# Optimization experiments

Hardware: AMD Instinct MI355X
Metric: run time of the kernel (lower is better)

Reference implementation:

```python
import jax, jax.numpy as jnp
import numpy as np

EPS = 1e-5  # torch nn.LayerNorm default eps
N_SUBJECTS = 16


def _gelu(x):
    # torch nn.GELU default = exact erf formulation
    return jax.nn.gelu(x, approximate=False)


def setup_inputs() -> dict:
    key = jax.random.key(0)
    ks = jax.random.split(key, 8)
    B, D = 131072, 512
    x = jax.random.normal(ks[0], (B, D), dtype=jnp.float32)
    groups = jax.random.randint(ks[1], (B,), 0, N_SUBJECTS, dtype=jnp.int32)
    # LayerNorm affine params: rows 0..15 subject-specific, row 16 = default_norm
    gammas = jnp.ones((N_SUBJECTS + 1, D), dtype=jnp.float32)
    betas = jnp.zeros((N_SUBJECTS + 1, D), dtype=jnp.float32)
    # Domain classifier MLP (xavier-uniform weights, zero biases)
    def xavier(k, fan_in, fan_out):
        lim = np.sqrt(6.0 / (fan_in + fan_out)).astype(np.float32)
        return jax.random.uniform(k, (fan_in, fan_out), dtype=jnp.float32,
                                  minval=-lim, maxval=lim)
    W1 = xavier(ks[2], D, 256); b1 = jnp.zeros((256,), jnp.float32)
    W2 = xavier(ks[3], 256, 128); b2 = jnp.zeros((128,), jnp.float32)
    W3 = xavier(ks[4], 128, N_SUBJECTS); b3 = jnp.zeros((N_SUBJECTS,), jnp.float32)
    return {"x": x, "groups": groups, "gammas": gammas, "betas": betas,
            "W1": W1, "b1": b1, "W2": W2, "b2": b2, "W3": W3, "b3": b3}


def _subject_layernorm(x, groups, gammas, betas):
    # Fused per-row LayerNorm with per-subject affine params.
    # Out-of-range subject ids (>= N_SUBJECTS or < 0) use the default row (index N_SUBJECTS).
    valid = (groups >= 0) & (groups < N_SUBJECTS)
    idx = jnp.where(valid, groups, N_SUBJECTS)
    g = gammas[idx]  # (B, D)
    b = betas[idx]   # (B, D)
    mu = jnp.mean(x, axis=-1, keepdims=True)
    var = jnp.mean(jnp.square(x - mu), axis=-1, keepdims=True)  # biased, as torch LN
    xn = (x - mu) * jax.lax.rsqrt(var + EPS)
    return xn * g + b


def _domain_classifier(x, W1, b1, W2, b2, W3, b3):
    # Dropout is identity in eval mode
    h = _gelu(x @ W1 + b1)
    h = _gelu(h @ W2 + b2)
    return h @ W3 + b3


def reference(x, groups, gammas, betas, W1, b1, W2, b2, W3, b3):
    # gradient reversal is identity in forward
    domain_logits = _domain_classifier(x, W1, b1, W2, b2, W3, b3)
    normalized_x = _subject_layernorm(x, groups, gammas, betas)
    return (normalized_x, domain_logits)
```

## Files before the change

### kernel.cpp

```cpp
#include <hip/hip_runtime.h>
#include <hip/hip_bf16.h>
#include <stdint.h>

#define NSUB 16

typedef short  bf16x8 __attribute__((ext_vector_type(8)));
typedef float  f32x4  __attribute__((ext_vector_type(4)));
typedef unsigned int u32x4 __attribute__((ext_vector_type(4)));

__device__ __forceinline__ float gelu_exact(float x){
  return 0.5f * x * (1.0f + erff(x * 0.70710678118654752440f));
}

__device__ __forceinline__ unsigned short f2bf(float f){
  union { float f; uint32_t u; } v; v.f = f;
  uint32_t u = v.u;
  return (unsigned short)((u + 0x7FFFu + ((u >> 16) & 1u)) >> 16);
}

__device__ __forceinline__ unsigned int pk2(float lo, float hi){
  union { __hip_bfloat162 b; unsigned int u; } c;
  c.b = __float22bfloat162_rn(make_float2(lo, hi));
  return c.u;
}

__device__ __forceinline__ bf16x8 as_bf(u32x4 v){
  union { u32x4 u; bf16x8 b; } c; c.u = v; return c.b;
}

__device__ __forceinline__ float bflo(unsigned int u){
  union { unsigned int u; float f; } c; c.u = u << 16; return c.f;
}
__device__ __forceinline__ float bfhi(unsigned int u){
  union { unsigned int u; float f; } c; c.u = u & 0xffff0000u; return c.f;
}

__global__ __launch_bounds__(256) void wconv_kernel(
    const float* __restrict__ W1, const float* __restrict__ W2, const float* __restrict__ W3,
    unsigned short* __restrict__ W1f, unsigned short* __restrict__ W2f, unsigned short* __restrict__ W3f){
  int t = blockIdx.x * 256 + threadIdx.x;
  if (t < 131072){
    int n = t >> 9, k = t & 511;
    int lane = ((k >> 3) & 3) * 16 + (n & 15);
    int idx = (((k >> 5) * 16 + (n >> 4)) * 64 + lane) * 8 + (k & 7);
    W1f[idx] = f2bf(W1[k*256 + n]);
  } else if (t < 131072 + 32768){
    int i = t - 131072; int n = i >> 8, k = i & 255;
    int lane = ((k >> 3) & 3) * 16 + (n & 15);
    int idx = (((k >> 5) * 8 + (n >> 4)) * 64 + lane) * 8 + (k & 7);
    W2f[idx] = f2bf(W2[k*128 + n]);
  } else if (t < 131072 + 32768 + 2048){
    int i = t - (131072 + 32768); int n = i >> 7, k = i & 127;
    int lane = ((k >> 3) & 3) * 16 + n;
    int idx = ((k >> 5) * 64 + lane) * 8 + (k & 7);
    W3f[idx] = f2bf(W3[k*16 + n]);
  }
}

__global__ __launch_bounds__(256) void fused_kernel(
    const float* __restrict__ x, const int* __restrict__ groups,
    const float* __restrict__ gammas, const float* __restrict__ betas,
    const unsigned short* __restrict__ W1f, const float* __restrict__ b1,
    const unsigned short* __restrict__ W2f, const float* __restrict__ b2,
    const unsigned short* __restrict__ W3f, const float* __restrict__ b3,
    float* __restrict__ ln_out, float* __restrict__ out2){
  __shared__ __align__(16) uint8_t smem[32768];
  constexpr int OFF_H2 = 16384;

  const int tid  = threadIdx.x;
  const int wave = tid >> 6;
  const int lane = tid & 63;
  const int l15  = lane & 15;
  const int g4   = lane >> 4;
  const int row0 = blockIdx.x * 32;

  const int sr  = tid >> 3;
  const int sc  = tid & 7;
  const int swz = (sr & 7) << 4;
  const int wb  = (sc*16) ^ swz;
  uint8_t* xrow = smem + sr*1024;
  const float* xg = x + (size_t)(row0 + sr)*512 + sc*8;

  float s = 0.f, q = 0.f;
  #pragma unroll
  for (int t = 0; t < 8; ++t){
    f32x4 v0 = *(const f32x4*)(xg + t*64);
    f32x4 v1 = *(const f32x4*)(xg + t*64 + 4);
    s += v0.x + v0.y + v0.z + v0.w + v1.x + v1.y + v1.z + v1.w;
    q += v0.x*v0.x + v0.y*v0.y + v0.z*v0.z + v0.w*v0.w
       + v1.x*v1.x + v1.y*v1.y + v1.z*v1.z + v1.w*v1.w;
    u32x4 pw;
    pw.x = pk2(v0.x, v0.y); pw.y = pk2(v0.z, v0.w);
    pw.z = pk2(v1.x, v1.y); pw.w = pk2(v1.z, v1.w);
    *(u32x4*)(xrow + t*128 + wb) = pw;
  }
  s += __shfl_xor(s, 1); s += __shfl_xor(s, 2); s += __shfl_xor(s, 4);
  q += __shfl_xor(q, 1); q += __shfl_xor(q, 2); q += __shfl_xor(q, 4);
  float mu  = s * (1.0f/512.0f);
  float var = q * (1.0f/512.0f) - mu*mu;
  float rs  = rsqrtf(var + 1e-5f);
  float nmr = -mu * rs;
  int gi   = groups[row0 + sr];
  int gidx = ((unsigned)gi < (unsigned)NSUB) ? gi : NSUB;

  float b1v[4], b2v[2], b3v;
  #pragma unroll
  for (int n = 0; n < 4; ++n) b1v[n] = b1[wave*64 + n*16 + l15];
  #pragma unroll
  for (int n = 0; n < 2; ++n) b2v[n] = b2[wave*32 + n*16 + l15];
  b3v = b3[l15];

  {
    const float* gpr = gammas + (size_t)gidx*512 + sc*8;
    const float* bpr = betas  + (size_t)gidx*512 + sc*8;
    float* op = ln_out + (size_t)(row0 + sr)*512 + sc*8;
    #pragma unroll
    for (int t = 0; t < 8; ++t){
      u32x4 pw = *(const u32x4*)(xrow + t*128 + wb);
      f32x4 g0 = *(const f32x4*)(gpr + t*64);
      f32x4 g1 = *(const f32x4*)(gpr + t*64 + 4);
      f32x4 e0 = *(const f32x4*)(bpr + t*64);
      f32x4 e1 = *(const f32x4*)(bpr + t*64 + 4);
      f32x4 o0, o1;
      o0.x = fmaf(fmaf(bflo(pw.x), rs, nmr), g0.x, e0.x);
      o0.y = fmaf(fmaf(bfhi(pw.x), rs, nmr), g0.y, e0.y);
      o0.z = fmaf(fmaf(bflo(pw.y), rs, nmr), g0.z, e0.z);
      o0.w = fmaf(fmaf(bfhi(pw.y), rs, nmr), g0.w, e0.w);
      o1.x = fmaf(fmaf(bflo(pw.z), rs, nmr), g1.x, e1.x);
      o1.y = fmaf(fmaf(bfhi(pw.z), rs, nmr), g1.y, e1.y);
      o1.z = fmaf(fmaf(bflo(pw.w), rs, nmr), g1.z, e1.z);
      o1.w = fmaf(fmaf(bfhi(pw.w), rs, nmr), g1.w, e1.w);
      *(f32x4*)(op + t*64)     = o0;
      *(f32x4*)(op + t*64 + 4) = o1;
    }
  }

  __syncthreads();

  int baseA[2][2];
  #pragma unroll
  for (int m = 0; m < 2; ++m){
    int row = m*16 + l15;
    int sw  = (row & 7) << 4;
    int bse = row*1024 + ((g4*16) ^ (sw & 0x30));
    int kx  = (row >> 2) & 1;
    baseA[m][0] = bse + ((0 ^ kx) << 6);
    baseA[m][1] = bse + ((1 ^ kx) << 6);
  }
  u32x4 braw[2][4];
  #pragma unroll
  for (int n = 0; n < 4; ++n)
    braw[0][n] = *(const u32x4*)(W1f + (size_t)(((wave*4 + n)*64 + lane)*8));
  f32x4 acc1[2][4] = {};
  #pragma unroll
  for (int g = 0; g < 16; ++g){
    if (g < 15){
      #pragma unroll
      for (int n = 0; n < 4; ++n)
        braw[(g+1)&1][n] = *(const u32x4*)(W1f + (size_t)((((g+1)*16 + wave*4 + n)*64 + lane)*8));
    }
    bf16x8 a[2];
    #pragma unroll
    for (int m = 0; m < 2; ++m)
      a[m] = *(const bf16x8*)(smem + baseA[m][g & 1] + (g >> 1)*128);
    #pragma unroll
    for (int m = 0; m < 2; ++m)
      #pragma unroll
      for (int n = 0; n < 4; ++n)
        acc1[m][n] = __builtin_amdgcn_mfma_f32_16x16x32_bf16(a[m], as_bf(braw[g & 1][n]), acc1[m][n], 0, 0, 0);
  }
  __syncthreads();

  u32x4 b2raw[2][2];
  #pragma unroll
  for (int n = 0; n < 2; ++n)
    b2raw[0][n] = *(const u32x4*)(W2f + (size_t)(((wave*2 + n)*64 + lane)*8));

  #pragma unroll
  for (int n = 0; n < 4; ++n){
    #pragma unroll
    for (int m = 0; m < 2; ++m){
      #pragma unroll
      for (int r = 0; r < 4; ++r){
        int row = m*16 + g4*4 + r;
        int col = wave*64 + n*16 + l15;
        float v = gelu_exact(acc1[m][n][r] + b1v[n]);
        *(unsigned short*)(smem + row*512 + ((col*2) ^ ((row & 7) << 4))) = f2bf(v);
      }
    }
  }
  __syncthreads();

  int baseH[2][2];
  #pragma unroll
  for (int m = 0; m < 2; ++m){
    int row = m*16 + l15;
    int sw  = (row & 7) << 4;
    int bse = row*512 + ((g4*16) ^ (sw & 0x30));
    int kx  = (row >> 2) & 1;
    baseH[m][0] = bse + ((0 ^ kx) << 6);
    baseH[m][1] = bse + ((1 ^ kx) << 6);
  }
  f32x4 acc2[2][2] = {};
  #pragma unroll
  for (int g = 0; g < 8; ++g){
    if (g < 7){
      #pragma unroll
      for (int n = 0; n < 2; ++n)
        b2raw[(g+1)&1][n] = *(const u32x4*)(W2f + (size_t)((((g+1)*8 + wave*2 + n)*64 + lane)*8));
    }
    bf16x8 a[2];
    #pragma unroll
    for (int m = 0; m < 2; ++m)
      a[m] = *(const bf16x8*)(smem + baseH[m][g & 1] + (g >> 1)*128);
    #pragma unroll
    for (int m = 0; m < 2; ++m)
      #pragma unroll
      for (int n = 0; n < 2; ++n)
        acc2[m][n] = __builtin_amdgcn_mfma_f32_16x16x32_bf16(a[m], as_bf(b2raw[g & 1][n]), acc2[m][n], 0, 0, 0);
  }

  u32x4 b3raw[4];
  #pragma unroll
  for (int ks = 0; ks < 4; ++ks)
    b3raw[ks] = *(const u32x4*)(W3f + (size_t)((ks*64 + lane)*8));

  #pragma unroll
  for (int n = 0; n < 2; ++n){
    #pragma unroll
    for (int m = 0; m < 2; ++m){
      #pragma unroll
      for (int r = 0; r < 4; ++r){
        int row = m*16 + g4*4 + r;
        int col = wave*32 + n*16 + l15;
        float v = gelu_exact(acc2[m][n][r] + b2v[n]);
        *(unsigned short*)(smem + OFF_H2 + row*256 + ((col*2) ^ ((row & 7) << 4))) = f2bf(v);
      }
    }
  }
  __syncthreads();

  int baseG[2];
  {
    int row = (wave & 1)*16 + l15;
    int sw  = (row & 7) << 4;
    int bse = OFF_H2 + row*256 + ((g4*16) ^ (sw & 0x30));
    int kx  = (row >> 2) & 1;
    baseG[0] = bse + ((0 ^ kx) << 6);
    baseG[1] = bse + ((1 ^ kx) << 6);
  }
  f32x4 acc3 = {};
  #pragma unroll
  for (int ks = 0; ks < 4; ++ks){
    bf16x8 a = *(const bf16x8*)(smem + baseG[ks & 1] + (ks >> 1)*128);
    acc3 = __builtin_amdgcn_mfma_f32_16x16x32_bf16(a, as_bf(b3raw[ks]), acc3, 0, 0, 0);
  }
  if (wave < 2){
    #pragma unroll
    for (int r = 0; r < 4; ++r){
      int grow = row0 + wave*16 + g4*4 + r;
      out2[(size_t)grow*16 + l15] = acc3[r] + b3v;
    }
  }
}

__global__ __launch_bounds__(256) void ln_kernel(
    const float* __restrict__ x, const int* __restrict__ groups,
    const float* __restrict__ gammas, const float* __restrict__ betas,
    float* __restrict__ out){
  int row  = blockIdx.x * 4 + (threadIdx.x >> 6);
  int lane = threadIdx.x & 63;
  const float4* xr = (const float4*)(x + (size_t)row * 512);
  float4 a = xr[lane];
  float4 b = xr[lane + 64];
  float s = a.x + a.y + a.z + a.w + b.x + b.y + b.z + b.w;
  float q = a.x*a.x + a.y*a.y + a.z*a.z + a.w*a.w
          + b.x*b.x + b.y*b.y + b.z*b.z + b.w*b.w;
  #pragma unroll
  for (int o = 32; o > 0; o >>= 1){
    s += __shfl_xor(s, o);
    q += __shfl_xor(q, o);
  }
  float mu  = s * (1.0f/512.0f);
  float var = q * (1.0f/512.0f) - mu*mu;
  float rs  = rsqrtf(var + 1e-5f);
  int gi = groups[row];
  int idx = ((unsigned)gi < (unsigned)NSUB) ? gi : NSUB;
  const float4* gr = (const float4*)(gammas + (size_t)idx * 512);
  const float4* br = (const float4*)(betas  + (size_t)idx * 512);
  float4 g0 = gr[lane], g1 = gr[lane + 64];
  float4 e0 = br[lane], e1 = br[lane + 64];
  float4 o0, o1;
  o0.x = (a.x - mu)*rs*g0.x + e0.x; o0.y = (a.y - mu)*rs*g0.y + e0.y;
  o0.z = (a.z - mu)*rs*g0.z + e0.z; o0.w = (a.w - mu)*rs*g0.w + e0.w;
  o1.x = (b.x - mu)*rs*g1.x + e1.x; o1.y = (b.y - mu)*rs*g1.y + e1.y;
  o1.z = (b.z - mu)*rs*g1.z + e1.z; o1.w = (b.w - mu)*rs*g1.w + e1.w;
  float4* orow = (float4*)(out + (size_t)row * 512);
  orow[lane]      = o0;
  orow[lane + 64] = o1;
}

__global__ __launch_bounds__(256) void mlp_naive(
    const float* __restrict__ x,
    const float* __restrict__ W1, const float* __restrict__ b1,
    const float* __restrict__ W2, const float* __restrict__ b2,
    const float* __restrict__ W3, const float* __restrict__ b3,
    float* __restrict__ out2){
  __shared__ float xr[512];
  __shared__ float h1[256];
  __shared__ float h2[128];
  int row = blockIdx.x, t = threadIdx.x;
  xr[t]       = x[(size_t)row*512 + t];
  xr[t + 256] = x[(size_t)row*512 + t + 256];
  __syncthreads();
  {
    float s = 0.f;
    for (int k = 0; k < 512; ++k) s += xr[k] * W1[k*256 + t];
    h1[t] = gelu_exact(s + b1[t]);
  }
  __syncthreads();
  if (t < 128){
    float s = 0.f;
    for (int k = 0; k < 256; ++k) s += h1[k] * W2[k*128 + t];
    h2[t] = gelu_exact(s + b2[t]);
  }
  __syncthreads();
  if (t < 16){
    float s = 0.f;
    for (int k = 0; k < 128; ++k) s += h2[k] * W3[k*16 + t];
    out2[(size_t)row*16 + t] = s + b3[t];
  }
}

extern "C" void kernel_launch(void* const* d_in, const int* in_sizes, int n_in,
                              void* d_out, int out_size, void* d_ws, size_t ws_size,
                              hipStream_t stream){
  const float* x      = (const float*)d_in[0];
  const int*   groups = (const int*)d_in[1];
  const float* gammas = (const float*)d_in[2];
  const float* betas  = (const float*)d_in[3];
  const float* W1 = (const float*)d_in[4];
  const float* b1 = (const float*)d_in[5];
  const float* W2 = (const float*)d_in[6];
  const float* b2 = (const float*)d_in[7];
  const float* W3 = (const float*)d_in[8];
  const float* b3 = (const float*)d_in[9];
  float* out  = (float*)d_out;
  const int B = in_sizes[0] / 512;
  float* out2 = out + (size_t)B * 512;

  const size_t ws_need = (size_t)(131072 + 32768 + 2048) * sizeof(unsigned short);
  if (ws_size >= ws_need){
    unsigned short* W1f = (unsigned short*)d_ws;
    unsigned short* W2f = W1f + 131072;
    unsigned short* W3f = W2f + 32768;
    int nconv = 131072 + 32768 + 2048;
    wconv_kernel<<<(nconv + 255)/256, 256, 0, stream>>>(W1, W2, W3, W1f, W2f, W3f);
    fused_kernel<<<B/32, 256, 0, stream>>>(x, groups, gammas, betas,
                                           W1f, b1, W2f, b2, W3f, b3, out, out2);
  } else {
    mlp_naive<<<B, 256, 0, stream>>>(x, W1, b1, W2, b2, W3, b3, out2);
    ln_kernel<<<B/4, 256, 0, stream>>>(x, groups, gammas, betas, out);
  }
}
```

Baseline: 189.2 us.

## Interleave LayerNorm output writes with first GEMM loop and use bf16 affine params

Moves the LayerNorm affine-output loop inside the first MFMA k-loop, so the per-row normalized stores overlap with matrix-core work instead of running before the barrier. Gammas and betas are now converted to bf16 in the prep kernel, which halves their gather traffic. W2 prefetch is deepened to three stages, output stores become nontemporal, and launch bounds request 4 blocks per CU. Rounding gamma and beta to bf16 adds error to the LayerNorm output. The extra register pressure from the deeper prefetch and the carried LN state may cause spills under the occupancy bound.

Result: no change. 188.1 us (-0.6%).

```diff
diff --git a/kernel.cpp b/kernel.cpp
--- a/kernel.cpp
+++ b/kernel.cpp
@@ -37,29 +37,38 @@
 
 __global__ __launch_bounds__(256) void wconv_kernel(
     const float* __restrict__ W1, const float* __restrict__ W2, const float* __restrict__ W3,
-    unsigned short* __restrict__ W1f, unsigned short* __restrict__ W2f, unsigned short* __restrict__ W3f){
+    const float* __restrict__ gammas, const float* __restrict__ betas,
+    unsigned short* __restrict__ W1f, unsigned short* __restrict__ W2f,
+    unsigned short* __restrict__ W3f, unsigned short* __restrict__ Gf,
+    unsigned short* __restrict__ Bf){
   int t = blockIdx.x * 256 + threadIdx.x;
   if (t < 131072){
     int n = t >> 9, k = t & 511;
     int lane = ((k >> 3) & 3) * 16 + (n & 15);
     int idx = (((k >> 5) * 16 + (n >> 4)) * 64 + lane) * 8 + (k & 7);
     W1f[idx] = f2bf(W1[k*256 + n]);
-  } else if (t < 131072 + 32768){
+  } else if (t < 163840){
     int i = t - 131072; int n = i >> 8, k = i & 255;
     int lane = ((k >> 3) & 3) * 16 + (n & 15);
     int idx = (((k >> 5) * 8 + (n >> 4)) * 64 + lane) * 8 + (k & 7);
     W2f[idx] = f2bf(W2[k*128 + n]);
-  } else if (t < 131072 + 32768 + 2048){
-    int i = t - (131072 + 32768); int n = i >> 7, k = i & 127;
+  } else if (t < 165888){
+    int i = t - 163840; int n = i >> 7, k = i & 127;
     int lane = ((k >> 3) & 3) * 16 + n;
     int idx = ((k >> 5) * 64 + lane) * 8 + (k & 7);
     W3f[idx] = f2bf(W3[k*16 + n]);
-  }
-}
-
-__global__ __launch_bounds__(256) void fused_kernel(
+  } else if (t < 174592){
+    int i = t - 165888;
+    Gf[i] = f2bf(gammas[i]);
+  } else if (t < 183296){
+    int i = t - 174592;
+    Bf[i] = f2bf(betas[i]);
+  }
+}
+
+__global__ __launch_bounds__(256, 4) void fused_kernel(
     const float* __restrict__ x, const int* __restrict__ groups,
-    const float* __restrict__ gammas, const float* __restrict__ betas,
+    const unsigned short* __restrict__ Gf, const unsigned short* __restrict__ Bf,
     const unsigned short* __restrict__ W1f, const float* __restrict__ b1,
     const unsigned short* __restrict__ W2f, const float* __restrict__ b2,
     const unsigned short* __restrict__ W3f, const float* __restrict__ b3,
@@ -80,6 +89,9 @@
   const int wb  = (sc*16) ^ swz;
   uint8_t* xrow = smem + sr*1024;
   const float* xg = x + (size_t)(row0 + sr)*512 + sc*8;
+
+  int gi   = groups[row0 + sr];
+  int gidx = ((unsigned)gi < (unsigned)NSUB) ? gi : NSUB;
 
   float s = 0.f, q = 0.f;
   #pragma unroll
@@ -100,8 +112,6 @@
   float var = q * (1.0f/512.0f) - mu*mu;
   float rs  = rsqrtf(var + 1e-5f);
   float nmr = -mu * rs;
-  int gi   = groups[row0 + sr];
-  int gidx = ((unsigned)gi < (unsigned)NSUB) ? gi : NSUB;
 
   float b1v[4], b2v[2], b3v;
   #pragma unroll
@@ -110,32 +120,17 @@
   for (int n = 0; n < 2; ++n) b2v[n] = b2[wave*32 + n*16 + l15];
   b3v = b3[l15];
 
-  {
-    const float* gpr = gammas + (size_t)gidx*512 + sc*8;
-    const float* bpr = betas  + (size_t)gidx*512 + sc*8;
-    float* op = ln_out + (size_t)(row0 + sr)*512 + sc*8;
-    #pragma unroll
-    for (int t = 0; t < 8; ++t){
-      u32x4 pw = *(const u32x4*)(xrow + t*128 + wb);
-      f32x4 g0 = *(const f32x4*)(gpr + t*64);
-      f32x4 g1 = *(const f32x4*)(gpr + t*64 + 4);
-      f32x4 e0 = *(const f32x4*)(bpr + t*64);
-      f32x4 e1 = *(const f32x4*)(bpr + t*64 + 4);
-      f32x4 o0, o1;
-      o0.x = fmaf(fmaf(bflo(pw.x), rs, nmr), g0.x, e0.x);
-      o0.y = fmaf(fmaf(bfhi(pw.x), rs, nmr), g0.y, e0.y);
-      o0.z = fmaf(fmaf(bflo(pw.y), rs, nmr), g0.z, e0.z);
-      o0.w = fmaf(fmaf(bfhi(pw.y), rs, nmr), g0.w, e0.w);
-      o1.x = fmaf(fmaf(bflo(pw.z), rs, nmr), g1.x, e1.x);
-      o1.y = fmaf(fmaf(bfhi(pw.z), rs, nmr), g1.y, e1.y);
-      o1.z = fmaf(fmaf(bflo(pw.w), rs, nmr), g1.z, e1.z);
-      o1.w = fmaf(fmaf(bfhi(pw.w), rs, nmr), g1.w, e1.w);
-      *(f32x4*)(op + t*64)     = o0;
-      *(f32x4*)(op + t*64 + 4) = o1;
-    }
-  }
-
-  __syncthreads();
+  const unsigned short* gam = Gf + (size_t)gidx*512 + sc*8;
+  const unsigned short* bet = Bf + (size_t)gidx*512 + sc*8;
+  float* op = ln_out + (size_t)(row0 + sr)*512 + sc*8;
+  u32x4 pwc = *(const u32x4*)(xrow + wb);
+  u32x4 ggc = *(const u32x4*)gam;
+  u32x4 bbc = *(const u32x4*)bet;
+
+  u32x4 braw[2][4];
+  #pragma unroll
+  for (int n = 0; n < 4; ++n)
+    braw[0][n] = *(const u32x4*)(W1f + (size_t)(((wave*4 + n)*64 + lane)*8));
 
   int baseA[2][2];
   #pragma unroll
@@ -147,10 +142,9 @@
     baseA[m][0] = bse + ((0 ^ kx) << 6);
     baseA[m][1] = bse + ((1 ^ kx) << 6);
   }
-  u32x4 braw[2][4];
-  #pragma unroll
-  for (int n = 0; n < 4; ++n)
-    braw[0][n] = *(const u32x4*)(W1f + (size_t)(((wave*4 + n)*64 + lane)*8));
+
+  __syncthreads();
+
   f32x4 acc1[2][4] = {};
   #pragma unroll
   for (int g = 0; g < 16; ++g){
@@ -163,18 +157,42 @@
     #pragma unroll
     for (int m = 0; m < 2; ++m)
       a[m] = *(const bf16x8*)(smem + baseA[m][g & 1] + (g >> 1)*128);
+    if (g & 1){
+      const int c = g >> 1;
+      u32x4 pwn = pwc, ggn = ggc, bbn = bbc;
+      if (c < 7){
+        pwn = *(const u32x4*)(xrow + (c+1)*128 + wb);
+        ggn = *(const u32x4*)(gam + (c+1)*64);
+        bbn = *(const u32x4*)(bet + (c+1)*64);
+      }
+      f32x4 o0, o1;
+      o0.x = fmaf(fmaf(bflo(pwc.x), rs, nmr), bflo(ggc.x), bflo(bbc.x));
+      o0.y = fmaf(fmaf(bfhi(pwc.x), rs, nmr), bfhi(ggc.x), bfhi(bbc.x));
+      o0.z = fmaf(fmaf(bflo(pwc.y), rs, nmr), bflo(ggc.y), bflo(bbc.y));
+      o0.w = fmaf(fmaf(bfhi(pwc.y), rs, nmr), bfhi(ggc.y), bfhi(bbc.y));
+      o1.x = fmaf(fmaf(bflo(pwc.z), rs, nmr), bflo(ggc.z), bflo(bbc.z));
+      o1.y = fmaf(fmaf(bfhi(pwc.z), rs, nmr), bfhi(ggc.z), bfhi(bbc.z));
+      o1.z = fmaf(fmaf(bflo(pwc.w), rs, nmr), bflo(ggc.w), bflo(bbc.w));
+      o1.w = fmaf(fmaf(bfhi(pwc.w), rs, nmr), bfhi(ggc.w), bfhi(bbc.w));
+      __builtin_nontemporal_store(o0, (f32x4*)(op + c*64));
+      __builtin_nontemporal_store(o1, (f32x4*)(op + c*64 + 4));
+      pwc = pwn; ggc = ggn; bbc = bbn;
+    }
     #pragma unroll
     for (int m = 0; m < 2; ++m)
       #pragma unroll
       for (int n = 0; n < 4; ++n)
         acc1[m][n] = __builtin_amdgcn_mfma_f32_16x16x32_bf16(a[m], as_bf(braw[g & 1][n]), acc1[m][n], 0, 0, 0);
   }
-  __syncthreads();
-
-  u32x4 b2raw[2][2];
-  #pragma unroll
-  for (int n = 0; n < 2; ++n)
-    b2raw[0][n] = *(const u32x4*)(W2f + (size_t)(((wave*2 + n)*64 + lane)*8));
+
+  u32x4 b2raw[4][2];
+  #pragma unroll
+  for (int p = 0; p < 3; ++p)
+    #pragma unroll
+    for (int n = 0; n < 2; ++n)
+      b2raw[p][n] = *(const u32x4*)(W2f + (size_t)(((p*8 + wave*2 + n)*64 + lane)*8));
+
+  __syncthreads();
 
   #pragma unroll
   for (int n = 0; n < 4; ++n){
@@ -204,10 +222,10 @@
   f32x4 acc2[2][2] = {};
   #pragma unroll
   for (int g = 0; g < 8; ++g){
-    if (g < 7){
+    if (g < 5){
       #pragma unroll
       for (int n = 0; n < 2; ++n)
-        b2raw[(g+1)&1][n] = *(const u32x4*)(W2f + (size_t)((((g+1)*8 + wave*2 + n)*64 + lane)*8));
+        b2raw[(g+3)&3][n] = *(const u32x4*)(W2f + (size_t)((((g+3)*8 + wave*2 + n)*64 + lane)*8));
     }
     bf16x8 a[2];
     #pragma unroll
@@ -217,7 +235,7 @@
     for (int m = 0; m < 2; ++m)
       #pragma unroll
       for (int n = 0; n < 2; ++n)
-        acc2[m][n] = __builtin_amdgcn_mfma_f32_16x16x32_bf16(a[m], as_bf(b2raw[g & 1][n]), acc2[m][n], 0, 0, 0);
+        acc2[m][n] = __builtin_amdgcn_mfma_f32_16x16x32_bf16(a[m], as_bf(b2raw[g & 3][n]), acc2[m][n], 0, 0, 0);
   }
 
   u32x4 b3raw[4];
@@ -259,7 +277,7 @@
     #pragma unroll
     for (int r = 0; r < 4; ++r){
       int grow = row0 + wave*16 + g4*4 + r;
-      out2[(size_t)grow*16 + l15] = acc3[r] + b3v;
+      __builtin_nontemporal_store(acc3[r] + b3v, &out2[(size_t)grow*16 + l15]);
     }
   }
 }
@@ -283,7 +301,7 @@
   }
   float mu  = s * (1.0f/512.0f);
   float var = q * (1.0f/512.0f) - mu*mu;
-  float rs  = rsqrtf(var + 1e-5f);
+  float rsq = rsqrtf(var + 1e-5f);
   int gi = groups[row];
   int idx = ((unsigned)gi < (unsigned)NSUB) ? gi : NSUB;
   const float4* gr = (const float4*)(gammas + (size_t)idx * 512);
@@ -291,10 +309,10 @@
   float4 g0 = gr[lane], g1 = gr[lane + 64];
   float4 e0 = br[lane], e1 = br[lane + 64];
   float4 o0, o1;
-  o0.x = (a.x - mu)*rs*g0.x + e0.x; o0.y = (a.y - mu)*rs*g0.y + e0.y;
-  o0.z = (a.z - mu)*rs*g0.z + e0.z; o0.w = (a.w - mu)*rs*g0.w + e0.w;
-  o1.x = (b.x - mu)*rs*g1.x + e1.x; o1.y = (b.y - mu)*rs*g1.y + e1.y;
-  o1.z = (b.z - mu)*rs*g1.z + e1.z; o1.w = (b.w - mu)*rs*g1.w + e1.w;
+  o0.x = (a.x - mu)*rsq*g0.x + e0.x; o0.y = (a.y - mu)*rsq*g0.y + e0.y;
+  o0.z = (a.z - mu)*rsq*g0.z + e0.z; o0.w = (a.w - mu)*rsq*g0.w + e0.w;
+  o1.x = (b.x - mu)*rsq*g1.x + e1.x; o1.y = (b.y - mu)*rsq*g1.y + e1.y;
+  o1.z = (b.z - mu)*rsq*g1.z + e1.z; o1.w = (b.w - mu)*rsq*g1.w + e1.w;
   float4* orow = (float4*)(out + (size_t)row * 512);
   orow[lane]      = o0;
   orow[lane + 64] = o1;
@@ -349,14 +367,17 @@
   const int B = in_sizes[0] / 512;
   float* out2 = out + (size_t)B * 512;
 
-  const size_t ws_need = (size_t)(131072 + 32768 + 2048) * sizeof(unsigned short);
+  const int n_u16 = 131072 + 32768 + 2048 + 8704 + 8704;
+  const size_t ws_need = (size_t)n_u16 * sizeof(unsigned short);
   if (ws_size >= ws_need){
     unsigned short* W1f = (unsigned short*)d_ws;
     unsigned short* W2f = W1f + 131072;
     unsigned short* W3f = W2f + 32768;
-    int nconv = 131072 + 32768 + 2048;
-    wconv_kernel<<<(nconv + 255)/256, 256, 0, stream>>>(W1, W2, W3, W1f, W2f, W3f);
-    fused_kernel<<<B/32, 256, 0, stream>>>(x, groups, gammas, betas,
+    unsigned short* Gf  = W3f + 2048;
+    unsigned short* Bf  = Gf + 8704;
+    wconv_kernel<<<(n_u16 + 255)/256, 256, 0, stream>>>(W1, W2, W3, gammas, betas,
+                                                        W1f, W2f, W3f, Gf, Bf);
+    fused_kernel<<<B/32, 256, 0, stream>>>(x, groups, Gf, Bf,
                                            W1f, b1, W2f, b2, W3f, b3, out, out2);
   } else {
     mlp_naive<<<B, 256, 0, stream>>>(x, W1, b1, W2, b2, W3, b3, out2);
```

## Halve rows per block, shrink LDS, deepen W2 prefetch, use fast GELU

Applied to the files above, without the earlier changes.

Processes 16 rows per block instead of 32, halving shared memory and per-wave accumulators so more blocks can be resident to hide memory latency. W2 fragments are prefetched three stages ahead, and the W1 prefetch is hoisted before the LayerNorm output. Exact erf GELU is replaced by a sigmoid-form tanh approximation built on exp2/rcp intrinsics. In exchange each block amortises weight loads over fewer rows, raising weight traffic, and the GELU becomes approximate.

Measured after the change: 221.4 us. +17.0%, slower.

```diff
diff --git a/kernel.cpp b/kernel.cpp
--- a/kernel.cpp
+++ b/kernel.cpp
@@ -10,6 +10,15 @@
 
 __device__ __forceinline__ float gelu_exact(float x){
   return 0.5f * x * (1.0f + erff(x * 0.70710678118654752440f));
+}
+
+__device__ __forceinline__ float gelu_fast(float x){
+  float xx = x * x;
+  float m  = fmaf(0.044715f, xx, 1.0f);
+  float a  = x * m * -2.3022084f;
+  float e  = __builtin_amdgcn_exp2f(a);
+  float r  = __builtin_amdgcn_rcpf(e + 1.0f);
+  return x * r;
 }
 
 __device__ __forceinline__ unsigned short f2bf(float f){
@@ -44,13 +53,13 @@
     int lane = ((k >> 3) & 3) * 16 + (n & 15);
     int idx = (((k >> 5) * 16 + (n >> 4)) * 64 + lane) * 8 + (k & 7);
     W1f[idx] = f2bf(W1[k*256 + n]);
-  } else if (t < 131072 + 32768){
+  } else if (t < 163840){
     int i = t - 131072; int n = i >> 8, k = i & 255;
     int lane = ((k >> 3) & 3) * 16 + (n & 15);
     int idx = (((k >> 5) * 8 + (n >> 4)) * 64 + lane) * 8 + (k & 7);
     W2f[idx] = f2bf(W2[k*128 + n]);
-  } else if (t < 131072 + 32768 + 2048){
-    int i = t - (131072 + 32768); int n = i >> 7, k = i & 127;
+  } else if (t < 165888){
+    int i = t - 163840; int n = i >> 7, k = i & 127;
     int lane = ((k >> 3) & 3) * 16 + n;
     int idx = ((k >> 5) * 64 + lane) * 8 + (k & 7);
     W3f[idx] = f2bf(W3[k*16 + n]);
@@ -64,44 +73,51 @@
     const unsigned short* __restrict__ W2f, const float* __restrict__ b2,
     const unsigned short* __restrict__ W3f, const float* __restrict__ b3,
     float* __restrict__ ln_out, float* __restrict__ out2){
-  __shared__ __align__(16) uint8_t smem[32768];
-  constexpr int OFF_H2 = 16384;
+  __shared__ __align__(16) uint8_t smem[16384];
+  constexpr int OFF_H2 = 8192;
 
   const int tid  = threadIdx.x;
   const int wave = tid >> 6;
   const int lane = tid & 63;
   const int l15  = lane & 15;
   const int g4   = lane >> 4;
-  const int row0 = blockIdx.x * 32;
-
-  const int sr  = tid >> 3;
-  const int sc  = tid & 7;
+  const int row0 = blockIdx.x * 16;
+
+  const int sr  = tid >> 4;
+  const int sc  = tid & 15;
   const int swz = (sr & 7) << 4;
-  const int wb  = (sc*16) ^ swz;
   uint8_t* xrow = smem + sr*1024;
   const float* xg = x + (size_t)(row0 + sr)*512 + sc*8;
 
+  int gi   = groups[row0 + sr];
+  int gidx = ((unsigned)gi < (unsigned)NSUB) ? gi : NSUB;
+
   float s = 0.f, q = 0.f;
   #pragma unroll
-  for (int t = 0; t < 8; ++t){
-    f32x4 v0 = *(const f32x4*)(xg + t*64);
-    f32x4 v1 = *(const f32x4*)(xg + t*64 + 4);
+  for (int c = 0; c < 4; ++c){
+    f32x4 v0 = *(const f32x4*)(xg + c*128);
+    f32x4 v1 = *(const f32x4*)(xg + c*128 + 4);
     s += v0.x + v0.y + v0.z + v0.w + v1.x + v1.y + v1.z + v1.w;
     q += v0.x*v0.x + v0.y*v0.y + v0.z*v0.z + v0.w*v0.w
        + v1.x*v1.x + v1.y*v1.y + v1.z*v1.z + v1.w*v1.w;
     u32x4 pw;
     pw.x = pk2(v0.x, v0.y); pw.y = pk2(v0.z, v0.w);
     pw.z = pk2(v1.x, v1.y); pw.w = pk2(v1.z, v1.w);
-    *(u32x4*)(xrow + t*128 + wb) = pw;
-  }
-  s += __shfl_xor(s, 1); s += __shfl_xor(s, 2); s += __shfl_xor(s, 4);
-  q += __shfl_xor(q, 1); q += __shfl_xor(q, 2); q += __shfl_xor(q, 4);
+    *(u32x4*)(xrow + ((c*256 + sc*16) ^ swz)) = pw;
+  }
+  s += __shfl_xor(s, 1); s += __shfl_xor(s, 2);
+  s += __shfl_xor(s, 4); s += __shfl_xor(s, 8);
+  q += __shfl_xor(q, 1); q += __shfl_xor(q, 2);
+  q += __shfl_xor(q, 4); q += __shfl_xor(q, 8);
   float mu  = s * (1.0f/512.0f);
   float var = q * (1.0f/512.0f) - mu*mu;
   float rs  = rsqrtf(var + 1e-5f);
   float nmr = -mu * rs;
-  int gi   = groups[row0 + sr];
-  int gidx = ((unsigned)gi < (unsigned)NSUB) ? gi : NSUB;
+
+  u32x4 braw[2][4];
+  #pragma unroll
+  for (int n = 0; n < 4; ++n)
+    braw[0][n] = *(const u32x4*)(W1f + (size_t)(((wave*4 + n)*64 + lane)*8));
 
   float b1v[4], b2v[2], b3v;
   #pragma unroll
@@ -115,12 +131,12 @@
     const float* bpr = betas  + (size_t)gidx*512 + sc*8;
     float* op = ln_out + (size_t)(row0 + sr)*512 + sc*8;
     #pragma unroll
-    for (int t = 0; t < 8; ++t){
-      u32x4 pw = *(const u32x4*)(xrow + t*128 + wb);
-      f32x4 g0 = *(const f32x4*)(gpr + t*64);
-      f32x4 g1 = *(const f32x4*)(gpr + t*64 + 4);
-      f32x4 e0 = *(const f32x4*)(bpr + t*64);
-      f32x4 e1 = *(const f32x4*)(bpr + t*64 + 4);
+    for (int c = 0; c < 4; ++c){
+      u32x4 pw = *(const u32x4*)(xrow + ((c*256 + sc*16) ^ swz));
+      f32x4 g0 = *(const f32x4*)(gpr + c*128);
+      f32x4 g1 = *(const f32x4*)(gpr + c*128 + 4);
+      f32x4 e0 = *(const f32x4*)(bpr + c*128);
+      f32x4 e1 = *(const f32x4*)(bpr + c*128 + 4);
       f32x4 o0, o1;
       o0.x = fmaf(fmaf(bflo(pw.x), rs, nmr), g0.x, e0.x);
       o0.y = fmaf(fmaf(bfhi(pw.x), rs, nmr), g0.y, e0.y);
@@ -130,28 +146,24 @@
       o1.y = fmaf(fmaf(bfhi(pw.z), rs, nmr), g1.y, e1.y);
       o1.z = fmaf(fmaf(bflo(pw.w), rs, nmr), g1.z, e1.z);
       o1.w = fmaf(fmaf(bfhi(pw.w), rs, nmr), g1.w, e1.w);
-      *(f32x4*)(op + t*64)     = o0;
-      *(f32x4*)(op + t*64 + 4) = o1;
-    }
-  }
-
-  __syncthreads();
-
-  int baseA[2][2];
-  #pragma unroll
-  for (int m = 0; m < 2; ++m){
-    int row = m*16 + l15;
+      *(f32x4*)(op + c*128)     = o0;
+      *(f32x4*)(op + c*128 + 4) = o1;
+    }
+  }
+
+  int baseA[2];
+  {
+    int row = l15;
     int sw  = (row & 7) << 4;
     int bse = row*1024 + ((g4*16) ^ (sw & 0x30));
     int kx  = (row >> 2) & 1;
-    baseA[m][0] = bse + ((0 ^ kx) << 6);
-    baseA[m][1] = bse + ((1 ^ kx) << 6);
-  }
-  u32x4 braw[2][4];
-  #pragma unroll
-  for (int n = 0; n < 4; ++n)
-    braw[0][n] = *(const u32x4*)(W1f + (size_t)(((wave*4 + n)*64 + lane)*8));
-  f32x4 acc1[2][4] = {};
+    baseA[0] = bse + ((0 ^ kx) << 6);
+    baseA[1] = bse + ((1 ^ kx) << 6);
+  }
+
+  __syncthreads();
+
+  f32x4 acc1[4] = {};
   #pragma unroll
   for (int g = 0; g < 16; ++g){
     if (g < 15){
@@ -159,65 +171,54 @@
       for (int n = 0; n < 4; ++n)
         braw[(g+1)&1][n] = *(const u32x4*)(W1f + (size_t)((((g+1)*16 + wave*4 + n)*64 + lane)*8));
     }
-    bf16x8 a[2];
-    #pragma unroll
-    for (int m = 0; m < 2; ++m)
-      a[m] = *(const bf16x8*)(smem + baseA[m][g & 1] + (g >> 1)*128);
-    #pragma unroll
-    for (int m = 0; m < 2; ++m)
-      #pragma unroll
-      for (int n = 0; n < 4; ++n)
-        acc1[m][n] = __builtin_amdgcn_mfma_f32_16x16x32_bf16(a[m], as_bf(braw[g & 1][n]), acc1[m][n], 0, 0, 0);
-  }
-  __syncthreads();
-
-  u32x4 b2raw[2][2];
-  #pragma unroll
-  for (int n = 0; n < 2; ++n)
-    b2raw[0][n] = *(const u32x4*)(W2f + (size_t)(((wave*2 + n)*64 + lane)*8));
+    bf16x8 a = *(const bf16x8*)(smem + baseA[g & 1] + (g >> 1)*128);
+    #pragma unroll
+    for (int n = 0; n < 4; ++n)
+      acc1[n] = __builtin_amdgcn_mfma_f32_16x16x32_bf16(a, as_bf(braw[g & 1][n]), acc1[n], 0, 0, 0);
+  }
+
+  u32x4 b2raw[4][2];
+  #pragma unroll
+  for (int p = 0; p < 3; ++p)
+    #pragma unroll
+    for (int n = 0; n < 2; ++n)
+      b2raw[p][n] = *(const u32x4*)(W2f + (size_t)(((p*8 + wave*2 + n)*64 + lane)*8));
+
+  __syncthreads();
 
   #pragma unroll
   for (int n = 0; n < 4; ++n){
     #pragma unroll
-    for (int m = 0; m < 2; ++m){
-      #pragma unroll
-      for (int r = 0; r < 4; ++r){
-        int row = m*16 + g4*4 + r;
-        int col = wave*64 + n*16 + l15;
-        float v = gelu_exact(acc1[m][n][r] + b1v[n]);
-        *(unsigned short*)(smem + row*512 + ((col*2) ^ ((row & 7) << 4))) = f2bf(v);
-      }
-    }
-  }
-  __syncthreads();
-
-  int baseH[2][2];
-  #pragma unroll
-  for (int m = 0; m < 2; ++m){
-    int row = m*16 + l15;
+    for (int r = 0; r < 4; ++r){
+      int row = g4*4 + r;
+      int col = wave*64 + n*16 + l15;
+      float v = gelu_fast(acc1[n][r] + b1v[n]);
+      *(unsigned short*)(smem + row*512 + ((col*2) ^ ((row & 7) << 4))) = f2bf(v);
+    }
+  }
+  __syncthreads();
+
+  int baseH[2];
+  {
+    int row = l15;
     int sw  = (row & 7) << 4;
     int bse = row*512 + ((g4*16) ^ (sw & 0x30));
     int kx  = (row >> 2) & 1;
-    baseH[m][0] = bse + ((0 ^ kx) << 6);
-    baseH[m][1] = bse + ((1 ^ kx) << 6);
-  }
-  f32x4 acc2[2][2] = {};
+    baseH[0] = bse + ((0 ^ kx) << 6);
+    baseH[1] = bse + ((1 ^ kx) << 6);
+  }
+  f32x4 acc2[2] = {};
   #pragma unroll
   for (int g = 0; g < 8; ++g){
-    if (g < 7){
+    if (g < 5){
       #pragma unroll
       for (int n = 0; n < 2; ++n)
-        b2raw[(g+1)&1][n] = *(const u32x4*)(W2f + (size_t)((((g+1)*8 + wave*2 + n)*64 + lane)*8));
-    }
-    bf16x8 a[2];
-    #pragma unroll
-    for (int m = 0; m < 2; ++m)
-      a[m] = *(const bf16x8*)(smem + baseH[m][g & 1] + (g >> 1)*128);
-    #pragma unroll
-    for (int m = 0; m < 2; ++m)
-      #pragma unroll
-      for (int n = 0; n < 2; ++n)
-        acc2[m][n] = __builtin_amdgcn_mfma_f32_16x16x32_bf16(a[m], as_bf(b2raw[g & 1][n]), acc2[m][n], 0, 0, 0);
+        b2raw[(g+3)&3][n] = *(const u32x4*)(W2f + (size_t)((((g+3)*8 + wave*2 + n)*64 + lane)*8));
+    }
+    bf16x8 a = *(const bf16x8*)(smem + baseH[g & 1] + (g >> 1)*128);
+    #pragma unroll
+    for (int n = 0; n < 2; ++n)
+      acc2[n] = __builtin_amdgcn_mfma_f32_16x16x32_bf16(a, as_bf(b2raw[g & 3][n]), acc2[n], 0, 0, 0);
   }
 
   u32x4 b3raw[4];
@@ -228,21 +229,18 @@
   #pragma unroll
   for (int n = 0; n < 2; ++n){
     #pragma unroll
-    for (int m = 0; m < 2; ++m){
-      #pragma unroll
-      for (int r = 0; r < 4; ++r){
-        int row = m*16 + g4*4 + r;
-        int col = wave*32 + n*16 + l15;
-        float v = gelu_exact(acc2[m][n][r] + b2v[n]);
-        *(unsigned short*)(smem + OFF_H2 + row*256 + ((col*2) ^ ((row & 7) << 4))) = f2bf(v);
-      }
+    for (int r = 0; r < 4; ++r){
+      int row = g4*4 + r;
+      int col = wave*32 + n*16 + l15;
+      float v = gelu_fast(acc2[n][r] + b2v[n]);
+      *(unsigned short*)(smem + OFF_H2 + row*256 + ((col*2) ^ ((row & 7) << 4))) = f2bf(v);
     }
   }
   __syncthreads();
 
   int baseG[2];
   {
-    int row = (wave & 1)*16 + l15;
+    int row = l15;
     int sw  = (row & 7) << 4;
     int bse = OFF_H2 + row*256 + ((g4*16) ^ (sw & 0x30));
     int kx  = (row >> 2) & 1;
@@ -255,10 +253,10 @@
     bf16x8 a = *(const bf16x8*)(smem + baseG[ks & 1] + (ks >> 1)*128);
     acc3 = __builtin_amdgcn_mfma_f32_16x16x32_bf16(a, as_bf(b3raw[ks]), acc3, 0, 0, 0);
   }
-  if (wave < 2){
+  if (wave == 0){
     #pragma unroll
     for (int r = 0; r < 4; ++r){
-      int grow = row0 + wave*16 + g4*4 + r;
+      int grow = row0 + g4*4 + r;
       out2[(size_t)grow*16 + l15] = acc3[r] + b3v;
     }
   }
@@ -283,7 +281,7 @@
   }
   float mu  = s * (1.0f/512.0f);
   float var = q * (1.0f/512.0f) - mu*mu;
-  float rs  = rsqrtf(var + 1e-5f);
+  float rsq = rsqrtf(var + 1e-5f);
   int gi = groups[row];
   int idx = ((unsigned)gi < (unsigned)NSUB) ? gi : NSUB;
   const float4* gr = (const float4*)(gammas + (size_t)idx * 512);
@@ -291,10 +289,10 @@
   float4 g0 = gr[lane], g1 = gr[lane + 64];
   float4 e0 = br[lane], e1 = br[lane + 64];
   float4 o0, o1;
-  o0.x = (a.x - mu)*rs*g0.x + e0.x; o0.y = (a.y - mu)*rs*g0.y + e0.y;
-  o0.z = (a.z - mu)*rs*g0.z + e0.z; o0.w = (a.w - mu)*rs*g0.w + e0.w;
-  o1.x = (b.x - mu)*rs*g1.x + e1.x; o1.y = (b.y - mu)*rs*g1.y + e1.y;
-  o1.z = (b.z - mu)*rs*g1.z + e1.z; o1.w = (b.w - mu)*rs*g1.w + e1.w;
+  o0.x = (a.x - mu)*rsq*g0.x + e0.x; o0.y = (a.y - mu)*rsq*g0.y + e0.y;
+  o0.z = (a.z - mu)*rsq*g0.z + e0.z; o0.w = (a.w - mu)*rsq*g0.w + e0.w;
+  o1.x = (b.x - mu)*rsq*g1.x + e1.x; o1.y = (b.y - mu)*rsq*g1.y + e1.y;
+  o1.z = (b.z - mu)*rsq*g1.z + e1.z; o1.w = (b.w - mu)*rsq*g1.w + e1.w;
   float4* orow = (float4*)(out + (size_t)row * 512);
   orow[lane]      = o0;
   orow[lane + 64] = o1;
@@ -349,14 +347,14 @@
   const int B = in_sizes[0] / 512;
   float* out2 = out + (size_t)B * 512;
 
-  const size_t ws_need = (size_t)(131072 + 32768 + 2048) * sizeof(unsigned short);
+  const int n_u16 = 131072 + 32768 + 2048;
+  const size_t ws_need = (size_t)n_u16 * sizeof(unsigned short);
   if (ws_size >= ws_need){
     unsigned short* W1f = (unsigned short*)d_ws;
     unsigned short* W2f = W1f + 131072;
     unsigned short* W3f = W2f + 32768;
-    int nconv = 131072 + 32768 + 2048;
-    wconv_kernel<<<(nconv + 255)/256, 256, 0, stream>>>(W1, W2, W3, W1f, W2f, W3f);
-    fused_kernel<<<B/32, 256, 0, stream>>>(x, groups, gammas, betas,
+    wconv_kernel<<<(n_u16 + 255)/256, 256, 0, stream>>>(W1, W2, W3, W1f, W2f, W3f);
+    fused_kernel<<<B/16, 256, 0, stream>>>(x, groups, gammas, betas,
                                            W1f, b1, W2f, b2, W3f, b3, out, out2);
   } else {
     mlp_naive<<<B, 256, 0, stream>>>(x, W1, b1, W2, b2, W3, b3, out2);
```

## Use 64-row blocks with 8 waves, deeper weight prefetch and tanh-form GELU

Applied to the files above, without the earlier changes.

The fused kernel now runs 512 threads per block over 64 rows instead of 256 threads over 32 rows. Each wave covers all four M tiles against fewer N columns, which doubles reuse of each streamed weight fragment, and the weight prefetch ring deepens from two to three or four stages. The exact erf GELU is replaced by a tanh/sigmoid approximation built on exp2 and rcp intrinsics, to cut the transcendental cost in the epilogues. In exchange, shared memory doubles to 64 KB, register pressure rises, and the GELU differs slightly from the exact erf form.

After: 155.5 us. 1.22x faster.

```diff
diff --git a/kernel.cpp b/kernel.cpp
--- a/kernel.cpp
+++ b/kernel.cpp
@@ -10,6 +10,15 @@
 
 __device__ __forceinline__ float gelu_exact(float x){
   return 0.5f * x * (1.0f + erff(x * 0.70710678118654752440f));
+}
+
+__device__ __forceinline__ float gelu_fast(float x){
+  float xx = x * x;
+  float m  = fmaf(0.044715f, xx, 1.0f);
+  float a  = x * m * -2.3022084f;
+  float e  = __builtin_amdgcn_exp2f(a);
+  float r  = __builtin_amdgcn_rcpf(e + 1.0f);
+  return x * r;
 }
 
 __device__ __forceinline__ unsigned short f2bf(float f){
@@ -44,35 +53,35 @@
     int lane = ((k >> 3) & 3) * 16 + (n & 15);
     int idx = (((k >> 5) * 16 + (n >> 4)) * 64 + lane) * 8 + (k & 7);
     W1f[idx] = f2bf(W1[k*256 + n]);
-  } else if (t < 131072 + 32768){
+  } else if (t < 163840){
     int i = t - 131072; int n = i >> 8, k = i & 255;
     int lane = ((k >> 3) & 3) * 16 + (n & 15);
     int idx = (((k >> 5) * 8 + (n >> 4)) * 64 + lane) * 8 + (k & 7);
     W2f[idx] = f2bf(W2[k*128 + n]);
-  } else if (t < 131072 + 32768 + 2048){
-    int i = t - (131072 + 32768); int n = i >> 7, k = i & 127;
+  } else if (t < 165888){
+    int i = t - 163840; int n = i >> 7, k = i & 127;
     int lane = ((k >> 3) & 3) * 16 + n;
     int idx = ((k >> 5) * 64 + lane) * 8 + (k & 7);
     W3f[idx] = f2bf(W3[k*16 + n]);
   }
 }
 
-__global__ __launch_bounds__(256) void fused_kernel(
+__global__ __launch_bounds__(512, 4) void fused_kernel(
     const float* __restrict__ x, const int* __restrict__ groups,
     const float* __restrict__ gammas, const float* __restrict__ betas,
     const unsigned short* __restrict__ W1f, const float* __restrict__ b1,
     const unsigned short* __restrict__ W2f, const float* __restrict__ b2,
     const unsigned short* __restrict__ W3f, const float* __restrict__ b3,
     float* __restrict__ ln_out, float* __restrict__ out2){
-  __shared__ __align__(16) uint8_t smem[32768];
-  constexpr int OFF_H2 = 16384;
+  __shared__ __align__(16) uint8_t smem[65536];
+  constexpr int OFF_H2 = 32768;
 
   const int tid  = threadIdx.x;
   const int wave = tid >> 6;
   const int lane = tid & 63;
   const int l15  = lane & 15;
   const int g4   = lane >> 4;
-  const int row0 = blockIdx.x * 32;
+  const int row0 = blockIdx.x * 64;
 
   const int sr  = tid >> 3;
   const int sc  = tid & 7;
@@ -80,6 +89,9 @@
   const int wb  = (sc*16) ^ swz;
   uint8_t* xrow = smem + sr*1024;
   const float* xg = x + (size_t)(row0 + sr)*512 + sc*8;
+
+  int gi   = groups[row0 + sr];
+  int gidx = ((unsigned)gi < (unsigned)NSUB) ? gi : NSUB;
 
   float s = 0.f, q = 0.f;
   #pragma unroll
@@ -100,15 +112,19 @@
   float var = q * (1.0f/512.0f) - mu*mu;
   float rs  = rsqrtf(var + 1e-5f);
   float nmr = -mu * rs;
-  int gi   = groups[row0 + sr];
-  int gidx = ((unsigned)gi < (unsigned)NSUB) ? gi : NSUB;
-
-  float b1v[4], b2v[2], b3v;
-  #pragma unroll
-  for (int n = 0; n < 4; ++n) b1v[n] = b1[wave*64 + n*16 + l15];
-  #pragma unroll
-  for (int n = 0; n < 2; ++n) b2v[n] = b2[wave*32 + n*16 + l15];
-  b3v = b3[l15];
+
+  u32x4 braw[4][2];
+  #pragma unroll
+  for (int p = 0; p < 3; ++p)
+    #pragma unroll
+    for (int n = 0; n < 2; ++n)
+      braw[p][n] = *(const u32x4*)(W1f + (size_t)(((p*16 + wave*2 + n)*64 + lane)*8));
+
+  float b1v[2];
+  #pragma unroll
+  for (int n = 0; n < 2; ++n) b1v[n] = b1[wave*32 + n*16 + l15];
+  float b2v = b2[wave*16 + l15];
+  float b3v = b3[l15];
 
   {
     const float* gpr = gammas + (size_t)gidx*512 + sc*8;
@@ -135,11 +151,9 @@
     }
   }
 
-  __syncthreads();
-
-  int baseA[2][2];
-  #pragma unroll
-  for (int m = 0; m < 2; ++m){
+  int baseA[4][2];
+  #pragma unroll
+  for (int m = 0; m < 4; ++m){
     int row = m*16 + l15;
     int sw  = (row & 7) << 4;
     int bse = row*1024 + ((g4*16) ^ (sw & 0x30));
@@ -147,53 +161,53 @@
     baseA[m][0] = bse + ((0 ^ kx) << 6);
     baseA[m][1] = bse + ((1 ^ kx) << 6);
   }
-  u32x4 braw[2][4];
-  #pragma unroll
-  for (int n = 0; n < 4; ++n)
-    braw[0][n] = *(const u32x4*)(W1f + (size_t)(((wave*4 + n)*64 + lane)*8));
-  f32x4 acc1[2][4] = {};
+
+  __syncthreads();
+
+  f32x4 acc1[4][2] = {};
   #pragma unroll
   for (int g = 0; g < 16; ++g){
-    if (g < 15){
+    if (g < 13){
       #pragma unroll
-      for (int n = 0; n < 4; ++n)
-        braw[(g+1)&1][n] = *(const u32x4*)(W1f + (size_t)((((g+1)*16 + wave*4 + n)*64 + lane)*8));
-    }
-    bf16x8 a[2];
-    #pragma unroll
-    for (int m = 0; m < 2; ++m)
+      for (int n = 0; n < 2; ++n)
+        braw[(g+3)&3][n] = *(const u32x4*)(W1f + (size_t)((((g+3)*16 + wave*2 + n)*64 + lane)*8));
+    }
+    bf16x8 a[4];
+    #pragma unroll
+    for (int m = 0; m < 4; ++m)
       a[m] = *(const bf16x8*)(smem + baseA[m][g & 1] + (g >> 1)*128);
     #pragma unroll
-    for (int m = 0; m < 2; ++m)
+    for (int m = 0; m < 4; ++m)
       #pragma unroll
-      for (int n = 0; n < 4; ++n)
-        acc1[m][n] = __builtin_amdgcn_mfma_f32_16x16x32_bf16(a[m], as_bf(braw[g & 1][n]), acc1[m][n], 0, 0, 0);
-  }
-  __syncthreads();
-
-  u32x4 b2raw[2][2];
-  #pragma unroll
-  for (int n = 0; n < 2; ++n)
-    b2raw[0][n] = *(const u32x4*)(W2f + (size_t)(((wave*2 + n)*64 + lane)*8));
-
-  #pragma unroll
-  for (int n = 0; n < 4; ++n){
-    #pragma unroll
-    for (int m = 0; m < 2; ++m){
+      for (int n = 0; n < 2; ++n)
+        acc1[m][n] = __builtin_amdgcn_mfma_f32_16x16x32_bf16(a[m], as_bf(braw[g & 3][n]), acc1[m][n], 0, 0, 0);
+  }
+
+  u32x4 b2raw[4];
+  #pragma unroll
+  for (int p = 0; p < 3; ++p)
+    b2raw[p] = *(const u32x4*)(W2f + (size_t)(((p*8 + wave)*64 + lane)*8));
+
+  __syncthreads();
+
+  #pragma unroll
+  for (int n = 0; n < 2; ++n){
+    #pragma unroll
+    for (int m = 0; m < 4; ++m){
       #pragma unroll
       for (int r = 0; r < 4; ++r){
         int row = m*16 + g4*4 + r;
-        int col = wave*64 + n*16 + l15;
-        float v = gelu_exact(acc1[m][n][r] + b1v[n]);
+        int col = wave*32 + n*16 + l15;
+        float v = gelu_fast(acc1[m][n][r] + b1v[n]);
         *(unsigned short*)(smem + row*512 + ((col*2) ^ ((row & 7) << 4))) = f2bf(v);
       }
     }
   }
   __syncthreads();
 
-  int baseH[2][2];
-  #pragma unroll
-  for (int m = 0; m < 2; ++m){
+  int baseH[4][2];
+  #pragma unroll
+  for (int m = 0; m < 4; ++m){
     int row = m*16 + l15;
     int sw  = (row & 7) << 4;
     int bse = row*512 + ((g4*16) ^ (sw & 0x30));
@@ -201,23 +215,18 @@
     baseH[m][0] = bse + ((0 ^ kx) << 6);
     baseH[m][1] = bse + ((1 ^ kx) << 6);
   }
-  f32x4 acc2[2][2] = {};
+  f32x4 acc2[4] = {};
   #pragma unroll
   for (int g = 0; g < 8; ++g){
-    if (g < 7){
-      #pragma unroll
-      for (int n = 0; n < 2; ++n)
-        b2raw[(g+1)&1][n] = *(const u32x4*)(W2f + (size_t)((((g+1)*8 + wave*2 + n)*64 + lane)*8));
-    }
-    bf16x8 a[2];
-    #pragma unroll
-    for (int m = 0; m < 2; ++m)
+    if (g < 5)
+      b2raw[(g+3)&3] = *(const u32x4*)(W2f + (size_t)((((g+3)*8 + wave)*64 + lane)*8));
+    bf16x8 a[4];
+    #pragma unroll
+    for (int m = 0; m < 4; ++m)
       a[m] = *(const bf16x8*)(smem + baseH[m][g & 1] + (g >> 1)*128);
     #pragma unroll
-    for (int m = 0; m < 2; ++m)
-      #pragma unroll
-      for (int n = 0; n < 2; ++n)
-        acc2[m][n] = __builtin_amdgcn_mfma_f32_16x16x32_bf16(a[m], as_bf(b2raw[g & 1][n]), acc2[m][n], 0, 0, 0);
+    for (int m = 0; m < 4; ++m)
+      acc2[m] = __builtin_amdgcn_mfma_f32_16x16x32_bf16(a[m], as_bf(b2raw[g & 3]), acc2[m], 0, 0, 0);
   }
 
   u32x4 b3raw[4];
@@ -226,36 +235,33 @@
     b3raw[ks] = *(const u32x4*)(W3f + (size_t)((ks*64 + lane)*8));
 
   #pragma unroll
-  for (int n = 0; n < 2; ++n){
-    #pragma unroll
-    for (int m = 0; m < 2; ++m){
-      #pragma unroll
-      for (int r = 0; r < 4; ++r){
-        int row = m*16 + g4*4 + r;
-        int col = wave*32 + n*16 + l15;
-        float v = gelu_exact(acc2[m][n][r] + b2v[n]);
-        *(unsigned short*)(smem + OFF_H2 + row*256 + ((col*2) ^ ((row & 7) << 4))) = f2bf(v);
-      }
-    }
-  }
-  __syncthreads();
-
-  int baseG[2];
-  {
-    int row = (wave & 1)*16 + l15;
-    int sw  = (row & 7) << 4;
-    int bse = OFF_H2 + row*256 + ((g4*16) ^ (sw & 0x30));
-    int kx  = (row >> 2) & 1;
-    baseG[0] = bse + ((0 ^ kx) << 6);
-    baseG[1] = bse + ((1 ^ kx) << 6);
-  }
-  f32x4 acc3 = {};
-  #pragma unroll
-  for (int ks = 0; ks < 4; ++ks){
-    bf16x8 a = *(const bf16x8*)(smem + baseG[ks & 1] + (ks >> 1)*128);
-    acc3 = __builtin_amdgcn_mfma_f32_16x16x32_bf16(a, as_bf(b3raw[ks]), acc3, 0, 0, 0);
-  }
-  if (wave < 2){
+  for (int m = 0; m < 4; ++m){
+    #pragma unroll
+    for (int r = 0; r < 4; ++r){
+      int row = m*16 + g4*4 + r;
+      int col = wave*16 + l15;
+      float v = gelu_fast(acc2[m][r] + b2v);
+      *(unsigned short*)(smem + OFF_H2 + row*256 + ((col*2) ^ ((row & 7) << 4))) = f2bf(v);
+    }
+  }
+  __syncthreads();
+
+  if (wave < 4){
+    int baseG[2];
+    {
+      int row = wave*16 + l15;
+      int sw  = (row & 7) << 4;
+      int bse = OFF_H2 + row*256 + ((g4*16) ^ (sw & 0x30));
+      int kx  = (row >> 2) & 1;
+      baseG[0] = bse + ((0 ^ kx) << 6);
+      baseG[1] = bse + ((1 ^ kx) << 6);
+    }
+    f32x4 acc3 = {};
+    #pragma unroll
+    for (int ks = 0; ks < 4; ++ks){
+      bf16x8 a = *(const bf16x8*)(smem + baseG[ks & 1] + (ks >> 1)*128);
+      acc3 = __builtin_amdgcn_mfma_f32_16x16x32_bf16(a, as_bf(b3raw[ks]), acc3, 0, 0, 0);
+    }
     #pragma unroll
     for (int r = 0; r < 4; ++r){
       int grow = row0 + wave*16 + g4*4 + r;
@@ -283,7 +289,7 @@
   }
   float mu  = s * (1.0f/512.0f);
   float var = q * (1.0f/512.0f) - mu*mu;
-  float rs  = rsqrtf(var + 1e-5f);
+  float rsq = rsqrtf(var + 1e-5f);
   int gi = groups[row];
   int idx = ((unsigned)gi < (unsigned)NSUB) ? gi : NSUB;
   const float4* gr = (const float4*)(gammas + (size_t)idx * 512);
@@ -291,10 +297,10 @@
   float4 g0 = gr[lane], g1 = gr[lane + 64];
   float4 e0 = br[lane], e1 = br[lane + 64];
   float4 o0, o1;
-  o0.x = (a.x - mu)*rs*g0.x + e0.x; o0.y = (a.y - mu)*rs*g0.y + e0.y;
-  o0.z = (a.z - mu)*rs*g0.z + e0.z; o0.w = (a.w - mu)*rs*g0.w + e0.w;
-  o1.x = (b.x - mu)*rs*g1.x + e1.x; o1.y = (b.y - mu)*rs*g1.y + e1.y;
-  o1.z = (b.z - mu)*rs*g1.z + e1.z; o1.w = (b.w - mu)*rs*g1.w + e1.w;
+  o0.x = (a.x - mu)*rsq*g0.x + e0.x; o0.y = (a.y - mu)*rsq*g0.y + e0.y;
+  o0.z = (a.z - mu)*rsq*g0.z + e0.z; o0.w = (a.w - mu)*rsq*g0.w + e0.w;
+  o1.x = (b.x - mu)*rsq*g1.x + e1.x; o1.y = (b.y - mu)*rsq*g1.y + e1.y;
+  o1.z = (b.z - mu)*rsq*g1.z + e1.z; o1.w = (b.w - mu)*rsq*g1.w + e1.w;
   float4* orow = (float4*)(out + (size_t)row * 512);
   orow[lane]      = o0;
   orow[lane + 64] = o1;
@@ -349,14 +355,14 @@
   const int B = in_sizes[0] / 512;
   float* out2 = out + (size_t)B * 512;
 
-  const size_t ws_need = (size_t)(131072 + 32768 + 2048) * sizeof(unsigned short);
+  const int n_u16 = 131072 + 32768 + 2048;
+  const size_t ws_need = (size_t)n_u16 * sizeof(unsigned short);
   if (ws_size >= ws_need){
     unsigned short* W1f = (unsigned short*)d_ws;
     unsigned short* W2f = W1f + 131072;
     unsigned short* W3f = W2f + 32768;
-    int nconv = 131072 + 32768 + 2048;
-    wconv_kernel<<<(nconv + 255)/256, 256, 0, stream>>>(W1, W2, W3, W1f, W2f, W3f);
-    fused_kernel<<<B/32, 256, 0, stream>>>(x, groups, gammas, betas,
+    wconv_kernel<<<(n_u16 + 255)/256, 256, 0, stream>>>(W1, W2, W3, W1f, W2f, W3f);
+    fused_kernel<<<B/64, 512, 0, stream>>>(x, groups, gammas, betas,
                                            W1f, b1, W2f, b2, W3f, b3, out, out2);
   } else {
     mlp_naive<<<B, 256, 0, stream>>>(x, W1, b1, W2, b2, W3, b3, out2);
```
